# Performance work log

Hardware: AMD Instinct MI355X
Metric: run time of the kernel (lower is better)

Reference implementation:

```python
import jax, jax.numpy as jnp
import numpy as np

B, S, D = 8, 2048, 64
NEG = -1e9


def setup_inputs() -> dict:
    key = jax.random.key(0)
    kq, kk, kv = jax.random.split(key, 3)
    return {
        "queries": jax.random.normal(kq, (B, S, D), dtype=jnp.float32),
        "keys": jax.random.normal(kk, (B, S, D), dtype=jnp.float32),
        "values": jax.random.normal(kv, (B, S, D), dtype=jnp.float32),
        "mask_q": jnp.ones((B, S), dtype=jnp.float32),
        "mask_k": jnp.ones((B, S), dtype=jnp.float32),
        "mask_v": jnp.ones((B, S), dtype=jnp.float32),
    }


def reference(queries, keys, values, mask_q, mask_k, mask_v):
    # scaled QK^T: [B, Sq, Sk]
    scaler = jnp.sqrt(jnp.asarray(queries.shape[-1], dtype=queries.dtype))
    scores = jnp.einsum("bqd,bkd->bqk", queries, keys) / scaler
    # additive padding mask from outer product of query/key masks
    padding_mask = mask_q[:, :, None] * mask_k[:, None, :]  # [B, Sq, Sk]
    scores = scores + (1.0 - padding_mask) * NEG
    attention_weights = jax.nn.softmax(scores, axis=-1)
    # mask values then weighted sum
    values = values * mask_v[:, :, None]
    output = jnp.einsum("bqk,bkd->bqd", attention_weights, values)
    return output
```

## Files before the change

### kernel.cpp

```cpp
#include <hip/hip_runtime.h>
#include <hip/hip_bf16.h>
#include <math.h>

#define BATCH 8
#define SEQ   2048
#define DIM   64
#define NEGC   (-1e9f)
#define LOG2E  1.4426950408889634f
#define QSC    (LOG2E / 8.0f)
#define NEGC2  (-1.4426950408889634e9f)

typedef short short8  __attribute__((ext_vector_type(8)));
typedef float f32x4   __attribute__((ext_vector_type(4)));
typedef float f32x16  __attribute__((ext_vector_type(16)));
typedef unsigned int uint2v __attribute__((ext_vector_type(2)));

#define MFMA32(a, b, c) __builtin_amdgcn_mfma_f32_32x32x16_bf16((a), (b), (c), 0, 0, 0)

__device__ __forceinline__ ushort f2bf(float x) {
    uint u = __float_as_uint(x);
    uint r = (u + 0x7fffu + ((u >> 16) & 1u)) >> 16;
    return (ushort)r;
}
__device__ __forceinline__ float bf2f(ushort h) {
    return __uint_as_float(((uint)h) << 16);
}

__global__ __launch_bounds__(256)
void prep_kv(const float* __restrict__ K, const float* __restrict__ V,
             const float* __restrict__ MV, ushort* __restrict__ ws) {
    __shared__ float raw[64 * 68];
    const int t    = threadIdx.x;
    const int b    = blockIdx.x & 7;
    const int rr   = blockIdx.x >> 3;
    const int tile = rr & 31;
    const int kv   = rr >> 5;
    ushort* wsI = ws + (size_t)(b * 32 + tile) * 8192;

    if (kv == 0) {
        const float* Kb = K + ((size_t)b * SEQ + tile * 64) * DIM;
#pragma unroll
        for (int u = 0; u < 4; u++) {
            int f = t + 256 * u, key = f >> 4, d4 = (f & 15) * 4;
            *(float4*)&raw[key * 68 + d4] = *(const float4*)(Kb + (size_t)f * 4);
        }
        __syncthreads();
#pragma unroll
        for (int u = 0; u < 2; u++) {
            int r = t + 256 * u;
            int mt = r >> 8, kc = (r >> 6) & 3, L = r & 63;
            int key = mt * 32 + (L & 31), d0 = kc * 16 + (L >> 5) * 8;
            float4 x0 = *(float4*)&raw[key * 68 + d0];
            float4 x1 = *(float4*)&raw[key * 68 + d0 + 4];
            float xs[8] = {x0.x, x0.y, x0.z, x0.w, x1.x, x1.y, x1.z, x1.w};
            short8 hv;
#pragma unroll
            for (int j = 0; j < 8; j++) hv[j] = (short)f2bf(xs[j]);
            *(short8*)(wsI + r * 8) = hv;
        }
    } else {
        const float* Vb  = V  + ((size_t)b * SEQ + tile * 64) * DIM;
        const float* MVb = MV + (size_t)b * SEQ + tile * 64;
#pragma unroll
        for (int u = 0; u < 4; u++) {
            int f = t + 256 * u, key = f >> 4, d4 = (f & 15) * 4;
            float4 x = *(const float4*)(Vb + (size_t)f * 4);
            float mv = MVb[key];
            x.x *= mv; x.y *= mv; x.z *= mv; x.w *= mv;
            *(float4*)&raw[key * 68 + d4] = x;
        }
        __syncthreads();
#pragma unroll
        for (int u = 0; u < 2; u++) {
            int r = t + 256 * u;
            int dt = r >> 8, kc = (r >> 6) & 3, L = r & 63;
            int d = dt * 32 + (L & 31), k0 = kc * 16 + (L >> 5) * 8;
            short8 ov;
#pragma unroll
            for (int j = 0; j < 8; j++) ov[j] = (short)f2bf(raw[(k0 + j) * 68 + d]);
            *(short8*)(wsI + 4096 + r * 8) = ov;
        }
    }
}

__global__ __launch_bounds__(512, 2)
void attn_fused(const float* __restrict__ Q, const float* __restrict__ MQ,
                const float* __restrict__ MK, const ushort* __restrict__ ws,
                float* __restrict__ O) {
    __shared__ __align__(16) float Msc[2][3][64][36];
    __shared__ __align__(16) float Oout[2][32][72];

    const int t    = threadIdx.x;
    const int w    = t >> 6;
    const int lane = t & 63;
    const int h    = lane >> 5;
    const int lm   = lane & 31;
    const int qg   = w & 1;
    const int ks   = w >> 1;

    const int b  = blockIdx.x & 7;
    const int qt = blockIdx.x >> 3;
    const int q  = qt * 64 + qg * 32 + lm;

    const float*  MKb = MK + (size_t)b * SEQ;
    const ushort* wsB = ws + (size_t)b * 32 * 8192;

    short8 qh[4], ql[4];
    {
        const float* Qr = Q + ((size_t)b * SEQ + q) * DIM;
#pragma unroll
        for (int kc = 0; kc < 4; kc++) {
            const float* p = Qr + kc * 16 + h * 8;
            float4 x0 = *(const float4*)p;
            float4 x1 = *(const float4*)(p + 4);
            float xs[8] = {x0.x, x0.y, x0.z, x0.w, x1.x, x1.y, x1.z, x1.w};
#pragma unroll
            for (int j = 0; j < 8; j++) {
                float v   = xs[j] * QSC;
                ushort hi = f2bf(v);
                ql[kc][j] = (short)f2bf(v - bf2f(hi));
                qh[kc][j] = (short)hi;
            }
        }
    }
    const float mq    = MQ[(size_t)b * SEQ + q];
    const float apen2 = NEGC2 * mq;

    float m = -1e30f, l = 0.0f;
    f32x16 ot0, ot1;
#pragma unroll
    for (int i = 0; i < 16; i++) { ot0[i] = 0.0f; ot1[i] = 0.0f; }

    auto loadch = [&](short8 (&kf)[4], short8 (&vf)[4], f32x4 (&bias)[4], int ch) {
        const int tt = ch >> 1, mt = ch & 1;
        const ushort* img = wsB + (size_t)tt * 8192;
#pragma unroll
        for (int kc = 0; kc < 4; kc++)
            kf[kc] = *(const short8*)(img + (((mt * 4 + kc) << 6) + lane) * 8);
#pragma unroll
        for (int u = 0; u < 4; u++) {
            const int dt = u >> 1, c = u & 1;
            vf[u] = *(const short8*)(img + 4096 + (((dt * 4 + mt * 2 + c) << 6) + lane) * 8);
        }
        const float* mkp = MKb + ch * 32 + h * 4;
#pragma unroll
        for (int v = 0; v < 4; v++) {
            f32x4 mk = *(const f32x4*)(mkp + v * 8);
#pragma unroll
            for (int c = 0; c < 4; c++) bias[v][c] = NEGC2 - apen2 * mk[c];
        }
    };

    auto step = [&](const short8 (&kf)[4], const short8 (&vf)[4],
                    const f32x4 (&bias)[4]) {
        f32x16 st;
#pragma unroll
        for (int i = 0; i < 16; i++) st[i] = 0.0f;
        __builtin_amdgcn_s_setprio(1);
#pragma unroll
        for (int kc = 0; kc < 4; kc++) {
            st = MFMA32(kf[kc], qh[kc], st);
            st = MFMA32(kf[kc], ql[kc], st);
        }
        __builtin_amdgcn_s_setprio(0);

        float sv[16];
#pragma unroll
        for (int v = 0; v < 4; v++)
#pragma unroll
            for (int c = 0; c < 4; c++)
                sv[v * 4 + c] = st[v * 4 + c] + bias[v][c];
        float t0 = fmaxf(fmaxf(sv[0],  sv[1]),  sv[2]);
        float t1 = fmaxf(fmaxf(sv[3],  sv[4]),  sv[5]);
        float t2 = fmaxf(fmaxf(sv[6],  sv[7]),  sv[8]);
        float t3 = fmaxf(fmaxf(sv[9],  sv[10]), sv[11]);
        float t4 = fmaxf(fmaxf(sv[12], sv[13]), sv[14]);
        float cm = fmaxf(fmaxf(fmaxf(t0, t1), t2),
                         fmaxf(fmaxf(t3, t4), sv[15]));
        cm = fmaxf(cm, __shfl_xor(cm, 32));
        if (!__all(cm <= m)) {
            float nm    = fmaxf(m, cm);
            float alpha = exp2f(m - nm);
            m = nm;
            l *= alpha;
            ot0 *= alpha; ot1 *= alpha;
        }
        float p[16];
#pragma unroll
        for (int i = 0; i < 16; i++) p[i] = exp2f(sv[i] - m);
        float s0 = (p[0] + p[1]) + (p[2] + p[3]);
        float s1 = (p[4] + p[5]) + (p[6] + p[7]);
        float s2 = (p[8] + p[9]) + (p[10] + p[11]);
        float s3 = (p[12] + p[13]) + (p[14] + p[15]);
        float cs = (s0 + s1) + (s2 + s3);
        cs += __shfl_xor(cs, 32);
        l += cs;

        uint g[4][2];
#pragma unroll
        for (int v = 0; v < 4; v++) {
            __hip_bfloat162 c0 = __float22bfloat162_rn(make_float2(p[v*4+0], p[v*4+1]));
            __hip_bfloat162 c1 = __float22bfloat162_rn(make_float2(p[v*4+2], p[v*4+3]));
            __builtin_memcpy(&g[v][0], &c0, 4);
            __builtin_memcpy(&g[v][1], &c1, 4);
        }
        uint2v ra = __builtin_amdgcn_permlane32_swap(g[0][0], g[1][0], false, false);
        uint2v rb = __builtin_amdgcn_permlane32_swap(g[0][1], g[1][1], false, false);
        uint2v rc = __builtin_amdgcn_permlane32_swap(g[2][0], g[3][0], false, false);
        uint2v rd = __builtin_amdgcn_permlane32_swap(g[2][1], g[3][1], false, false);
        uint pbw[2][4] = {{ra[0], rb[0], ra[1], rb[1]},
                          {rc[0], rd[0], rc[1], rd[1]}};

        __builtin_amdgcn_s_setprio(1);
#pragma unroll
        for (int c = 0; c < 2; c++) {
            short8 pb;
            __builtin_memcpy(&pb, &pbw[c][0], 16);
            ot0 = MFMA32(vf[c],     pb, ot0);
            ot1 = MFMA32(vf[2 + c], pb, ot1);
        }
        __builtin_amdgcn_s_setprio(0);
    };

    short8 kA[4], vA[4], kB[4], vB[4];
    f32x4  bA[4], bB[4];
    const int ch0 = ks * 16;
    loadch(kA, vA, bA, ch0);
#pragma unroll 1
    for (int i = 0; i < 8; i++) {
        loadch(kB, vB, bB, ch0 + 2 * i + 1);
        step(kA, vA, bA);
        if (i < 7) loadch(kA, vA, bA, ch0 + 2 * i + 2);
        step(kB, vB, bB);
    }

    if (ks != 0) {
        float* sc = &Msc[qg][ks - 1][lane][0];
#pragma unroll
        for (int i = 0; i < 4; i++) {
            f32x4 r0, r1;
#pragma unroll
            for (int c = 0; c < 4; c++) { r0[c] = ot0[i*4+c]; r1[c] = ot1[i*4+c]; }
            *(f32x4*)&sc[i * 4]      = r0;
            *(f32x4*)&sc[16 + i * 4] = r1;
        }
        sc[32] = m;
        sc[33] = l;
    }
    __syncthreads();
    if (ks == 0) {
#pragma unroll
        for (int pp = 0; pp < 3; pp++) {
            const float* sc = &Msc[qg][pp][lane][0];
            float mb = sc[32], lb = sc[33];
            float nm = fmaxf(m, mb);
            float fa = exp2f(m - nm), fb = exp2f(mb - nm);
            m = nm;
            l = l * fa + lb * fb;
#pragma unroll
            for (int i = 0; i < 16; i++) {
                ot0[i] = ot0[i] * fa + sc[i] * fb;
                ot1[i] = ot1[i] * fa + sc[16 + i] * fb;
            }
        }
        const float inv = 1.0f / l;
#pragma unroll
        for (int dt = 0; dt < 2; dt++)
#pragma unroll
            for (int rq = 0; rq < 4; rq++) {
                f32x4 r;
#pragma unroll
                for (int c = 0; c < 4; c++)
                    r[c] = (dt ? ot1[rq * 4 + c] : ot0[rq * 4 + c]) * inv;
                *(f32x4*)&Oout[qg][lm][dt * 32 + rq * 8 + h * 4] = r;
            }
    }
    __syncthreads();

    float* Ob = O + ((size_t)b * SEQ + qt * 64) * DIM;
#pragma unroll
    for (int u = 0; u < 2; u++) {
        int f = t + 512 * u;
        int row = f >> 4, d4 = (f & 15) * 4;
        f32x4 val = *(const f32x4*)&Oout[row >> 5][row & 31][d4];
        *(f32x4*)(Ob + (size_t)row * DIM + d4) = val;
    }
}

extern "C" void kernel_launch(void* const* d_in, const int* in_sizes, int n_in,
                              void* d_out, int out_size, void* d_ws, size_t ws_size,
                              hipStream_t stream) {
    const float* Q  = (const float*)d_in[0];
    const float* K  = (const float*)d_in[1];
    const float* V  = (const float*)d_in[2];
    const float* MQ = (const float*)d_in[3];
    const float* MK = (const float*)d_in[4];
    const float* MV = (const float*)d_in[5];
    float* O = (float*)d_out;

    ushort* wsKV = (ushort*)d_ws;

    prep_kv   <<<dim3(512), dim3(256), 0, stream>>>(K, V, MV, wsKV);
    attn_fused<<<dim3(256), dim3(512), 0, stream>>>(Q, MQ, MK, wsKV, O);
}
```

Before: 99.97 us.

## Software-pipeline QK^T of next chunk ahead of softmax/PV of current chunk

```diff
diff --git a/kernel.cpp b/kernel.cpp
--- a/kernel.cpp
+++ b/kernel.cpp
@@ -131,12 +131,16 @@
 #pragma unroll
     for (int i = 0; i < 16; i++) { ot0[i] = 0.0f; ot1[i] = 0.0f; }
 
-    auto loadch = [&](short8 (&kf)[4], short8 (&vf)[4], f32x4 (&bias)[4], int ch) {
+    auto loadK = [&](short8 (&kf)[4], int ch) {
         const int tt = ch >> 1, mt = ch & 1;
         const ushort* img = wsB + (size_t)tt * 8192;
 #pragma unroll
         for (int kc = 0; kc < 4; kc++)
             kf[kc] = *(const short8*)(img + (((mt * 4 + kc) << 6) + lane) * 8);
+    };
+    auto loadVB = [&](short8 (&vf)[4], f32x4 (&bias)[4], int ch) {
+        const int tt = ch >> 1, mt = ch & 1;
+        const ushort* img = wsB + (size_t)tt * 8192;
 #pragma unroll
         for (int u = 0; u < 4; u++) {
             const int dt = u >> 1, c = u & 1;
@@ -151,19 +155,22 @@
         }
     };
 
-    auto step = [&](const short8 (&kf)[4], const short8 (&vf)[4],
+    auto qkt = [&](f32x16& st, const short8 (&kf)[4]) {
+        f32x16 s;
+#pragma unroll
+        for (int i = 0; i < 16; i++) s[i] = 0.0f;
+        __builtin_amdgcn_s_setprio(1);
+#pragma unroll
+        for (int kc = 0; kc < 4; kc++) {
+            s = MFMA32(kf[kc], qh[kc], s);
+            s = MFMA32(kf[kc], ql[kc], s);
+        }
+        __builtin_amdgcn_s_setprio(0);
+        st = s;
+    };
+
+    auto smpv = [&](const f32x16& st, const short8 (&vf)[4],
                     const f32x4 (&bias)[4]) {
-        f32x16 st;
-#pragma unroll
-        for (int i = 0; i < 16; i++) st[i] = 0.0f;
-        __builtin_amdgcn_s_setprio(1);
-#pragma unroll
-        for (int kc = 0; kc < 4; kc++) {
-            st = MFMA32(kf[kc], qh[kc], st);
-            st = MFMA32(kf[kc], ql[kc], st);
-        }
-        __builtin_amdgcn_s_setprio(0);
-
         float sv[16];
 #pragma unroll
         for (int v = 0; v < 4; v++)
@@ -224,15 +231,25 @@
 
     short8 kA[4], vA[4], kB[4], vB[4];
     f32x4  bA[4], bB[4];
+    f32x16 stA, stB;
     const int ch0 = ks * 16;
-    loadch(kA, vA, bA, ch0);
+    loadK(kA, ch0); loadVB(vA, bA, ch0); loadK(kB, ch0 + 1);
+    qkt(stA, kA);
 #pragma unroll 1
-    for (int i = 0; i < 8; i++) {
-        loadch(kB, vB, bB, ch0 + 2 * i + 1);
-        step(kA, vA, bA);
-        if (i < 7) loadch(kA, vA, bA, ch0 + 2 * i + 2);
-        step(kB, vB, bB);
-    }
+    for (int i = 0; i < 7; i++) {
+        loadVB(vB, bB, ch0 + 2 * i + 1);
+        qkt(stB, kB);
+        loadK(kA, ch0 + 2 * i + 2);
+        smpv(stA, vA, bA);
+        loadVB(vA, bA, ch0 + 2 * i + 2);
+        qkt(stA, kA);
+        loadK(kB, ch0 + 2 * i + 3);
+        smpv(stB, vB, bB);
+    }
+    loadVB(vB, bB, ch0 + 15);
+    qkt(stB, kB);
+    smpv(stA, vA, bA);
+    smpv(stB, vB, bB);
 
     if (ks != 0) {
         float* sc = &Msc[qg][ks - 1][lane][0];
```

Result: faster. 96.99 us (-3.0%).
